# Kernel tuning notes

Measured on AMD Instinct MI355X. Metric: run time of the kernel, lower is better.

Reference implementation:

```python
import jax, jax.numpy as jnp
import numpy as np

D_MODEL = 1024
NUM_HEADS = 16
ROPE_BASE = 10000.0


def _rope_sincos(T, head_dim, dtype):
    # angles[t, i] = t / base**(2i/head_dim), i in [0, head_dim//2)
    pos = jnp.arange(T, dtype=jnp.float32)[:, None]              # [T, 1]
    inv_freq = 1.0 / (ROPE_BASE ** (jnp.arange(0, head_dim, 2, dtype=jnp.float32) / head_dim))
    angles = pos * inv_freq                                       # [T, half]
    sin = jnp.sin(angles).astype(dtype)[None, :, None, :]         # [1, T, 1, half]
    cos = jnp.cos(angles).astype(dtype)[None, :, None, :]
    return sin, cos


def _apply_rope(x, sin, cos):
    # x: [B, T, H, head_dim]; deinterleave even/odd lanes, rotate, concat halves
    x1, x2 = x[..., ::2], x[..., 1::2]                            # [B, T, H, half] each
    return jnp.concatenate([x1 * cos - x2 * sin, x1 * sin + x2 * cos], axis=-1)


def setup_inputs() -> dict:
    key = jax.random.key(0)
    ks = jax.random.split(key, 5)
    B, T, D = 2, 2048, D_MODEL
    s = 0.02
    return {
        "x": jax.random.normal(ks[0], (B, T, D), dtype=jnp.float32),
        "w_qkv": jax.random.normal(ks[1], (3 * D, D), dtype=jnp.float32) * s,
        "b_qkv": jnp.zeros((3 * D,), dtype=jnp.float32),
        "w_out": jax.random.normal(ks[2], (D, D), dtype=jnp.float32) * s,
        "b_out": jnp.zeros((D,), dtype=jnp.float32),
    }


def reference(x, w_qkv, b_qkv, w_out, b_out):
    B, T, D = x.shape
    H = NUM_HEADS
    hd = D // H
    scale = hd ** -0.5

    qkv = (x @ w_qkv.T + b_qkv).reshape(B, T, 3, H, hd)
    q, k, v = qkv[:, :, 0], qkv[:, :, 1], qkv[:, :, 2]            # [B, T, H, hd]

    sin, cos = _rope_sincos(T, hd, x.dtype)
    q = _apply_rope(q, sin, cos)
    k = _apply_rope(k, sin, cos)

    scores = jnp.einsum("bthd,bshd->bhts", q, k) * scale          # [B, H, T, T]
    weights = jax.nn.softmax(scores, axis=-1)
    out = jnp.einsum("bhts,bshd->bthd", weights, v)               # [B, T, H, hd]
    out = out.reshape(B, T, D)
    return out @ w_out.T + b_out
```

## Files before the change

### kernel.cpp

```cpp
#include <hip/hip_runtime.h>
#include <cstdint>
#include <cstddef>

typedef __attribute__((ext_vector_type(8))) short short8;
typedef __attribute__((ext_vector_type(8))) __bf16 bf16x8;
typedef __attribute__((ext_vector_type(4))) float f32x4;
typedef __attribute__((ext_vector_type(16))) float f32x16;
typedef __attribute__((ext_vector_type(4))) unsigned int uint32x4;

#define LOG2E 1.44269504088896340736f

__device__ __forceinline__ unsigned short f2bf(float f) {
    unsigned int u = __builtin_bit_cast(unsigned int, f);
    u += 0x7fffu + ((u >> 16) & 1u);
    return (unsigned short)(u >> 16);
}

__device__ __forceinline__ f32x4 zero4() {
    f32x4 z; z.x = 0.f; z.y = 0.f; z.z = 0.f; z.w = 0.f; return z;
}
__device__ __forceinline__ f32x16 zero16() {
    f32x16 z;
    #pragma unroll
    for (int i = 0; i < 16; ++i) z[i] = 0.f;
    return z;
}

__device__ __forceinline__ f32x4 mfma16(short8 a, short8 b, f32x4 c) {
    return __builtin_amdgcn_mfma_f32_16x16x32_bf16(
        __builtin_bit_cast(bf16x8, a), __builtin_bit_cast(bf16x8, b), c, 0, 0, 0);
}
__device__ __forceinline__ f32x16 mfma32(short8 a, short8 b, f32x16 c) {
    return __builtin_amdgcn_mfma_f32_32x32x16_bf16(
        __builtin_bit_cast(bf16x8, a), __builtin_bit_cast(bf16x8, b), c, 0, 0, 0);
}

__device__ __forceinline__ unsigned int cvt_pk_bf16(float lo, float hi) {
    unsigned int r;
    asm("v_cvt_pk_bf16_f32 %0, %1, %2" : "=v"(r) : "v"(lo), "v"(hi));
    return r;
}

__device__ __forceinline__ uint2 permswap(unsigned x, unsigned y) {
#if __has_builtin(__builtin_amdgcn_permlane32_swap)
    auto r = __builtin_amdgcn_permlane32_swap(x, y, false, false);
    return make_uint2(r[0], r[1]);
#else
    int lane = threadIdx.x & 63;
    unsigned sy = __shfl_xor(y, 32), sx = __shfl_xor(x, 32);
    return make_uint2((lane < 32) ? x : sy, (lane < 32) ? sx : y);
#endif
}
__device__ __forceinline__ float red_max32(float v) {
    unsigned u = __builtin_bit_cast(unsigned, v);
    uint2 p = permswap(u, u);
    return fmaxf(__builtin_bit_cast(float, p.x), __builtin_bit_cast(float, p.y));
}

__device__ __forceinline__ void gload_lds16(const void* g, void* l, int lane) {
#if __has_builtin(__builtin_amdgcn_global_load_lds)
    __builtin_amdgcn_global_load_lds(
        (const __attribute__((address_space(1))) void*)g,
        (__attribute__((address_space(3))) void*)l, 16, 0, 0);
    (void)lane;
#else
    reinterpret_cast<int4*>(l)[lane] = *reinterpret_cast<const int4*>(g);
#endif
}

__global__ __launch_bounds__(256) void prep_kernel(
    const float* __restrict__ x, const float* __restrict__ wq,
    const float* __restrict__ wo,
    unsigned short* __restrict__ xb, unsigned short* __restrict__ wqb,
    unsigned short* __restrict__ wob, float2* __restrict__ tab) {
    const int S0 = 1048576, S1 = 786432, S2 = 262144;
    int i = blockIdx.x * 256 + threadIdx.x;
    const float* src; unsigned short* dst; int j;
    if (i < S0) { src = x; dst = xb; j = i; }
    else if (i < S0 + S1) { src = wq; dst = wqb; j = i - S0; }
    else if (i < S0 + S1 + S2) { src = wo; dst = wob; j = i - S0 - S1; }
    else {
        int idx = i - (S0 + S1 + S2);
        if (idx < 2048 * 32) {
            int t = idx >> 5, ii = idx & 31;
            float inv_freq = powf(10000.0f, -(float)ii / 32.0f);
            float ang = (float)t * inv_freq;
            tab[idx] = make_float2(cosf(ang), sinf(ang));
        }
        return;
    }
    float4 v = reinterpret_cast<const float4*>(src)[j];
    ushort4 o;
    o.x = f2bf(v.x); o.y = f2bf(v.y); o.z = f2bf(v.z); o.w = f2bf(v.w);
    reinterpret_cast<ushort4*>(dst)[j] = o;
}

template<int BM, int BN, int WMG, int WNG>
__device__ __forceinline__ void gemm_mainloop(
    const unsigned short* __restrict__ A, const unsigned short* __restrict__ B,
    int K, int m0, int n0, char* As, char* Bs,
    f32x4 (&acc)[BM / (WMG * 16)][BN / (WNG * 16)]) {
    constexpr int MT = BM / (WMG * 16), NTT = BN / (WNG * 16);
    constexpr int CA = BM / 64, CB = BN / 64;
    constexpr int ABUF = BM * 128, BBUF = BN * 128;
    int tid = threadIdx.x;
    int wave = tid >> 6, lane = tid & 63;
    int wm = wave / WNG, wn = wave % WNG;
    int g = lane >> 4, c = lane & 15;
    const int NS = K >> 6;

    auto stage = [&](int buf, int k0) {
        #pragma unroll
        for (int i = 0; i < CA; ++i) {
            int call = wave * CA + i;
            int s = call * 64 + lane;
            int row = s >> 3, c8 = s & 7;
            int csw = (c8 ^ (row & 7)) << 3;
            gload_lds16(A + (size_t)(m0 + row) * K + k0 + csw,
                        As + buf * ABUF + call * 1024, lane);
        }
        #pragma unroll
        for (int i = 0; i < CB; ++i) {
            int call = wave * CB + i;
            int s = call * 64 + lane;
            int row = s >> 3, c8 = s & 7;
            int csw = (c8 ^ (row & 7)) << 3;
            gload_lds16(B + (size_t)(n0 + row) * K + k0 + csw,
                        Bs + buf * BBUF + call * 1024, lane);
        }
    };

    stage(0, 0);

    #pragma unroll 1
    for (int t = 0; t < NS; ++t) {
        int cur = t & 1;
        asm volatile("s_waitcnt vmcnt(0)" ::: "memory");
        __builtin_amdgcn_s_barrier();
        __builtin_amdgcn_sched_barrier(0);
        if (t + 1 < NS) stage(cur ^ 1, (t + 1) * 64);

        const char* Ac = As + cur * ABUF;
        const char* Bc = Bs + cur * BBUF;
        #pragma unroll
        for (int kg = 0; kg < 2; ++kg) {
            short8 af[MT], bfr[NTT];
            #pragma unroll
            for (int mt = 0; mt < MT; ++mt) {
                int row = wm * (BM / WMG) + mt * 16 + c;
                af[mt] = *reinterpret_cast<const short8*>(Ac +
                    ((row * 128 + kg * 64 + g * 16) ^ ((row & 7) << 4)));
            }
            #pragma unroll
            for (int nt = 0; nt < NTT; ++nt) {
                int row = wn * (BN / WNG) + nt * 16 + c;
                bfr[nt] = *reinterpret_cast<const short8*>(Bc +
                    ((row * 128 + kg * 64 + g * 16) ^ ((row & 7) << 4)));
            }
            __builtin_amdgcn_s_setprio(1);
            #pragma unroll
            for (int mt = 0; mt < MT; ++mt)
                #pragma unroll
                for (int nt = 0; nt < NTT; ++nt)
                    acc[mt][nt] = mfma16(af[mt], bfr[nt], acc[mt][nt]);
            __builtin_amdgcn_s_setprio(0);
        }
    }
}

__global__ __launch_bounds__(512, 2) void qkv_gemm_kernel(
    const unsigned short* __restrict__ X, const unsigned short* __restrict__ W,
    const float* __restrict__ bias, const float2* __restrict__ tab,
    unsigned short* __restrict__ q, unsigned short* __restrict__ k,
    unsigned short* __restrict__ vt) {
    __shared__ char smem[80 * 1024];
    const int K = 1024;
    const float SCL = 0.125f * LOG2E;
    int flat = blockIdx.x;
    int swzb = (flat & 7) * 64 + (flat >> 3);
    int m0 = (swzb >> 4) * 128, n0 = (swzb & 15) * 192;
    f32x4 acc[2][6];
    #pragma unroll
    for (int i = 0; i < 2; ++i)
        #pragma unroll
        for (int j = 0; j < 6; ++j) acc[i][j] = zero4();

    gemm_mainloop<128, 192, 4, 2>(X, W, K, m0, n0, smem, smem + 32768, acc);

    int tid = threadIdx.x;
    int wave = tid >> 6, lane = tid & 63;
    int wm = wave >> 1, wn = wave & 1;
    int g = lane >> 4, c = lane & 15;
    int mbase = m0 + wm * 32, nbase = n0 + wn * 96;
    #pragma unroll
    for (int mt = 0; mt < 2; ++mt) {
        #pragma unroll
        for (int nt = 0; nt < 6; ++nt) {
            f32x4 a = acc[mt][nt];
            int n = nbase + nt * 16 + c;
            int s = n >> 10;
            int h = (n >> 6) & 15;
            int d = n & 63;
            float bn = bias[n];
            #pragma unroll
            for (int r = 0; r < 4; ++r) {
                int m = mbase + mt * 16 + g * 4 + r;
                int bb = m >> 11, t = m & 2047;
                float val = a[r] + bn;
                float partner = __shfl_xor(val, 1);
                int bh = bb * 16 + h;
                if (s == 2) {
                    vt[((size_t)bh * 64 + d) * 2048 + t] = f2bf(val);
                } else {
                    int i2 = d >> 1;
                    float2 cs = tab[t * 32 + i2];
                    float outv; int dout;
                    if ((d & 1) == 0) { outv = val * cs.x - partner * cs.y; dout = i2; }
                    else              { outv = partner * cs.y + val * cs.x; dout = 32 + i2; }
                    if (s == 0) outv *= SCL;
                    (s == 0 ? q : k)[((size_t)bh * 2048 + t) * 64 + dout] = f2bf(outv);
                }
            }
        }
    }
}

__global__ __launch_bounds__(512, 2) void attn_kernel(
    const unsigned short* __restrict__ Q, const unsigned short* __restrict__ Kin,
    const unsigned short* __restrict__ VT, unsigned short* __restrict__ O) {
    __shared__ int4 smem4[65536 / 16];
    char* smem = (char*)smem4;
    const int T = 2048, NT = 16;
    int flat = blockIdx.x + 16 * blockIdx.y;
    int swzb = (flat & 7) * 64 + (flat >> 3);
    int bh = swzb >> 4;
    int qt = swzb & 15;
    int tid = threadIdx.x, wave = tid >> 6, lane = tid & 63;
    int lam = lane & 31, hi = lane >> 5;
    int pair = wave & 3, half = wave >> 2;
    int q = qt * 128 + pair * 32 + lam;

    const unsigned short* Qb = Q + ((size_t)bh * T + q) * 64;
    const unsigned short* Kb = Kin + (size_t)bh * T * 64;
    const unsigned short* VTb = VT + (size_t)bh * 64 * T;

    uint32x4 qtmp[4];
    #pragma unroll
    for (int c4 = 0; c4 < 4; ++c4)
        qtmp[c4] = *reinterpret_cast<const uint32x4*>(Qb + c4 * 16 + hi * 8);
    #pragma unroll
    for (int c4 = 0; c4 < 4; ++c4)
        asm volatile("" : "+v"(qtmp[c4]));
    short8 qf[4];
    #pragma unroll
    for (int c4 = 0; c4 < 4; ++c4) qf[c4] = __builtin_bit_cast(short8, qtmp[c4]);

    short8 ones;
    #pragma unroll
    for (int i = 0; i < 8; ++i) ones[i] = (short)0x3F80;

    f32x16 o0 = zero16(), o1 = zero16(), lacc = zero16();
    float m_run = -1e30f;
    int swz = (lam & 7) << 4;

    char* Ks0 = smem + half * 16384;
    char* Vs0 = smem + 32768 + half * 16384;

    auto stage = [&](int buf, int t) {
        int j0 = half * 1024 + t * 64;
        #pragma unroll
        for (int i = 0; i < 2; ++i) {
            int call = pair * 2 + i;
            int s = call * 64 + lane;
            int row = s >> 3, c8 = s & 7;
            int csw = (c8 ^ (row & 7)) << 3;
            gload_lds16(Kb + (size_t)(j0 + row) * 64 + csw,
                        Ks0 + buf * 8192 + call * 1024, lane);
            gload_lds16(VTb + (size_t)row * T + j0 + csw,
                        Vs0 + buf * 8192 + call * 1024, lane);
        }
    };

    stage(0, 0);

    #pragma unroll 1
    for (int t = 0; t < NT; ++t) {
        int cur = t & 1;
        asm volatile("s_waitcnt vmcnt(0)" ::: "memory");
        __builtin_amdgcn_s_barrier();
        __builtin_amdgcn_sched_barrier(0);
        if (t + 1 < NT) stage(cur ^ 1, t + 1);

        const char* Kc = Ks0 + cur * 8192;
        const char* Vc = Vs0 + cur * 8192;

        f32x16 s0 = zero16(), s1 = zero16();
        __builtin_amdgcn_s_setprio(1);
        #pragma unroll
        for (int c4 = 0; c4 < 4; ++c4) {
            int col = c4 * 32 + hi * 16;
            short8 kf0 = *reinterpret_cast<const short8*>(Kc + ((lam * 128 + col) ^ swz));
            s0 = mfma32(kf0, qf[c4], s0);
            short8 kf1 = *reinterpret_cast<const short8*>(Kc + (((lam + 32) * 128 + col) ^ swz));
            s1 = mfma32(kf1, qf[c4], s1);
        }
        __builtin_amdgcn_s_setprio(0);

        float tm = fmaxf(s0[0], s1[0]);
        #pragma unroll
        for (int r = 1; r < 16; ++r) tm = fmaxf(tm, fmaxf(s0[r], s1[r]));
        float tmax = red_max32(tm);
        if (__any(tmax - m_run > 8.0f)) {
            float mnew = fmaxf(m_run, tmax);
            float alpha = exp2f(m_run - mnew);
            m_run = mnew;
            #pragma unroll
            for (int r = 0; r < 16; ++r) {
                o0[r] *= alpha; o1[r] *= alpha; lacc[r] *= alpha;
            }
        }
        float p0[16], p1[16];
        #pragma unroll
        for (int r = 0; r < 16; ++r) p0[r] = exp2f(s0[r] - m_run);
        #pragma unroll
        for (int r = 0; r < 16; ++r) p1[r] = exp2f(s1[r] - m_run);

        short8 pa[4];
        #pragma unroll
        for (int blk = 0; blk < 2; ++blk) {
            const float* p = blk ? p1 : p0;
            #pragma unroll
            for (int jt = 0; jt < 2; ++jt) {
                unsigned a0 = cvt_pk_bf16(p[jt * 8 + 0], p[jt * 8 + 1]);
                unsigned a1 = cvt_pk_bf16(p[jt * 8 + 2], p[jt * 8 + 3]);
                unsigned b0 = cvt_pk_bf16(p[jt * 8 + 4], p[jt * 8 + 5]);
                unsigned b1 = cvt_pk_bf16(p[jt * 8 + 6], p[jt * 8 + 7]);
                uint2 pr0 = permswap(a0, b0);
                uint2 pr1 = permswap(a1, b1);
                uint4 w;
                w.x = pr0.x;
                w.y = pr1.x;
                w.z = pr0.y;
                w.w = pr1.y;
                pa[blk * 2 + jt] = __builtin_bit_cast(short8, w);
            }
        }

        __builtin_amdgcn_s_setprio(1);
        #pragma unroll
        for (int jt = 0; jt < 4; ++jt) {
            int col = jt * 32 + hi * 16;
            short8 vf0 = *reinterpret_cast<const short8*>(Vc + ((lam * 128 + col) ^ swz));
            o0 = mfma32(vf0, pa[jt], o0);
            short8 vf1 = *reinterpret_cast<const short8*>(Vc + (((lam + 32) * 128 + col) ^ swz));
            o1 = mfma32(vf1, pa[jt], o1);
            lacc = mfma32(ones, pa[jt], lacc);
        }
        __builtin_amdgcn_s_setprio(0);
    }

    float l_run = lacc[0];

    __syncthreads();
    float* pb = (float*)(smem + pair * 8704);
    if (half) {
        #pragma unroll
        for (int r = 0; r < 16; ++r) {
            pb[lane * 34 + r] = o0[r];
            pb[lane * 34 + 16 + r] = o1[r];
        }
        pb[lane * 34 + 32] = m_run;
        pb[lane * 34 + 33] = l_run;
    }
    __syncthreads();
    if (half) return;

    float mb = pb[lane * 34 + 32], lb = pb[lane * 34 + 33];
    float m = fmaxf(m_run, mb);
    float wa = exp2f(m_run - m), wb = exp2f(mb - m);
    float l = l_run * wa + lb * wb;
    float rinv = 1.0f / l;
    #pragma unroll
    for (int r = 0; r < 16; ++r) {
        o0[r] = o0[r] * wa + pb[lane * 34 + r] * wb;
        o1[r] = o1[r] * wa + pb[lane * 34 + 16 + r] * wb;
    }

    int b_ = bh >> 4, h_ = bh & 15;
    unsigned short* Orow = O + ((size_t)(b_ * 2048) + q) * 1024 + h_ * 64;
    #pragma unroll
    for (int rq = 0; rq < 4; ++rq) {
        ushort4 w0, w1;
        w0.x = f2bf(o0[rq * 4 + 0] * rinv);
        w0.y = f2bf(o0[rq * 4 + 1] * rinv);
        w0.z = f2bf(o0[rq * 4 + 2] * rinv);
        w0.w = f2bf(o0[rq * 4 + 3] * rinv);
        w1.x = f2bf(o1[rq * 4 + 0] * rinv);
        w1.y = f2bf(o1[rq * 4 + 1] * rinv);
        w1.z = f2bf(o1[rq * 4 + 2] * rinv);
        w1.w = f2bf(o1[rq * 4 + 3] * rinv);
        int d0 = rq * 8 + hi * 4;
        *reinterpret_cast<ushort4*>(Orow + d0) = w0;
        *reinterpret_cast<ushort4*>(Orow + 32 + d0) = w1;
    }
}

__global__ __launch_bounds__(512, 2) void out_gemm_kernel(
    const unsigned short* __restrict__ Aattn, const unsigned short* __restrict__ W,
    const float* __restrict__ bias, float* __restrict__ out) {
    __shared__ char smem[48 * 1024];
    const int K = 1024, N = 1024;
    int flat = blockIdx.x;
    int swzb = (flat & 7) * 64 + (flat >> 3);
    int m0 = (swzb & 63) * 64, n0 = (swzb >> 6) * 128;
    f32x4 acc[2][2];
    #pragma unroll
    for (int i = 0; i < 2; ++i)
        #pragma unroll
        for (int j = 0; j < 2; ++j) acc[i][j] = zero4();

    gemm_mainloop<64, 128, 2, 4>(Aattn, W, K, m0, n0, smem, smem + 16384, acc);

    int tid = threadIdx.x;
    int wave = tid >> 6, lane = tid & 63;
    int wm = wave >> 2, wn = wave & 3;
    int g = lane >> 4, c = lane & 15;
    int mbase = m0 + wm * 32, nbase = n0 + wn * 32;
    #pragma unroll
    for (int mt = 0; mt < 2; ++mt)
        #pragma unroll
        for (int nt = 0; nt < 2; ++nt) {
            int n = nbase + nt * 16 + c;
            float bn = bias[n];
            #pragma unroll
            for (int r = 0; r < 4; ++r) {
                int m = mbase + mt * 16 + g * 4 + r;
                out[(size_t)m * N + n] = acc[mt][nt][r] + bn;
            }
        }
}

extern "C" void kernel_launch(void* const* d_in, const int* in_sizes, int n_in,
                              void* d_out, int out_size, void* d_ws, size_t ws_size,
                              hipStream_t stream) {
    (void)in_sizes; (void)n_in; (void)out_size; (void)ws_size;
    const float* x     = (const float*)d_in[0];
    const float* w_qkv = (const float*)d_in[1];
    const float* b_qkv = (const float*)d_in[2];
    const float* w_out = (const float*)d_in[3];
    const float* b_out = (const float*)d_in[4];
    float* out = (float*)d_out;

    const int B = 2, T = 2048, D = 1024;
    const int M = B * T;
    const size_t MB = 1024 * 1024;
    (void)D; (void)M;

    char* ws = (char*)d_ws;
    unsigned short* xb    = (unsigned short*)(ws);
    unsigned short* wqkvb = (unsigned short*)(ws + 8 * MB);
    unsigned short* woutb = (unsigned short*)(ws + 14 * MB);
    unsigned short* qb    = (unsigned short*)(ws + 16 * MB);
    unsigned short* kb    = (unsigned short*)(ws + 24 * MB);
    unsigned short* vtb   = (unsigned short*)(ws + 32 * MB);
    unsigned short* attnb = (unsigned short*)(ws + 40 * MB);
    float2* tab           = (float2*)(ws + 48 * MB);

    prep_kernel<<<dim3((2097152 + 65536) / 256), dim3(256), 0, stream>>>(
        x, w_qkv, w_out, xb, wqkvb, woutb, tab);
    qkv_gemm_kernel<<<dim3(512), dim3(512), 0, stream>>>(xb, wqkvb, b_qkv, tab, qb, kb, vtb);
    attn_kernel<<<dim3(T / 128, B * 16), dim3(512), 0, stream>>>(qb, kb, vtb, attnb);
    out_gemm_kernel<<<dim3(512), dim3(512), 0, stream>>>(attnb, woutb, b_out, out);
}
```

Baseline: 143.9 us.

## Drop KV split across wave halves; use 4 waves processing full KV sequence

The attention kernel previously used 8 waves, with two halves each covering half of the key/value sequence, and then merged the partial softmax states through shared memory. It now uses 4 waves per block. Each wave walks the full sequence in 128-key tiles, handled as two 64-key subtiles, so the cross-half merge and its extra barriers go away. In exchange, each block has half the waves and each wave does twice the sequential work, which reduces latency hiding unless occupancy makes up for it.

```diff
diff --git a/kernel.cpp b/kernel.cpp
--- a/kernel.cpp
+++ b/kernel.cpp
@@ -225,7 +225,7 @@
     }
 }
 
-__global__ __launch_bounds__(512, 2) void attn_kernel(
+__global__ __launch_bounds__(256, 2) void attn_kernel(
     const unsigned short* __restrict__ Q, const unsigned short* __restrict__ Kin,
     const unsigned short* __restrict__ VT, unsigned short* __restrict__ O) {
     __shared__ int4 smem4[65536 / 16];
@@ -237,8 +237,7 @@
     int qt = swzb & 15;
     int tid = threadIdx.x, wave = tid >> 6, lane = tid & 63;
     int lam = lane & 31, hi = lane >> 5;
-    int pair = wave & 3, half = wave >> 2;
-    int q = qt * 128 + pair * 32 + lam;
+    int q = qt * 128 + wave * 32 + lam;
 
     const unsigned short* Qb = Q + ((size_t)bh * T + q) * 64;
     const unsigned short* Kb = Kin + (size_t)bh * T * 64;
@@ -263,37 +262,28 @@
     float m_run = -1e30f;
     int swz = (lam & 7) << 4;
 
-    char* Ks0 = smem + half * 16384;
-    char* Vs0 = smem + 32768 + half * 16384;
+    char* KsB = smem;
+    char* VsB = smem + 32768;
 
     auto stage = [&](int buf, int t) {
-        int j0 = half * 1024 + t * 64;
-        #pragma unroll
-        for (int i = 0; i < 2; ++i) {
-            int call = pair * 2 + i;
-            int s = call * 64 + lane;
-            int row = s >> 3, c8 = s & 7;
-            int csw = (c8 ^ (row & 7)) << 3;
-            gload_lds16(Kb + (size_t)(j0 + row) * 64 + csw,
-                        Ks0 + buf * 8192 + call * 1024, lane);
-            gload_lds16(VTb + (size_t)row * T + j0 + csw,
-                        Vs0 + buf * 8192 + call * 1024, lane);
+        int j0 = t * 128;
+        #pragma unroll
+        for (int st = 0; st < 2; ++st) {
+            #pragma unroll
+            for (int i = 0; i < 2; ++i) {
+                int call = wave * 2 + i;
+                int s = call * 64 + lane;
+                int row = s >> 3, c8 = s & 7;
+                int csw = (c8 ^ (row & 7)) << 3;
+                gload_lds16(Kb + (size_t)(j0 + st * 64 + row) * 64 + csw,
+                            KsB + buf * 16384 + st * 8192 + call * 1024, lane);
+                gload_lds16(VTb + (size_t)row * T + j0 + st * 64 + csw,
+                            VsB + buf * 16384 + st * 8192 + call * 1024, lane);
+            }
         }
     };
 
-    stage(0, 0);
-
-    #pragma unroll 1
-    for (int t = 0; t < NT; ++t) {
-        int cur = t & 1;
-        asm volatile("s_waitcnt vmcnt(0)" ::: "memory");
-        __builtin_amdgcn_s_barrier();
-        __builtin_amdgcn_sched_barrier(0);
-        if (t + 1 < NT) stage(cur ^ 1, t + 1);
-
-        const char* Kc = Ks0 + cur * 8192;
-        const char* Vc = Vs0 + cur * 8192;
-
+    auto subtile = [&](const char* Kc, const char* Vc) {
         f32x16 s0 = zero16(), s1 = zero16();
         __builtin_amdgcn_s_setprio(1);
         #pragma unroll
@@ -357,35 +347,25 @@
             lacc = mfma32(ones, pa[jt], lacc);
         }
         __builtin_amdgcn_s_setprio(0);
+    };
+
+    stage(0, 0);
+
+    #pragma unroll 1
+    for (int t = 0; t < NT; ++t) {
+        int cur = t & 1;
+        asm volatile("s_waitcnt vmcnt(0)" ::: "memory");
+        __builtin_amdgcn_s_barrier();
+        __builtin_amdgcn_sched_barrier(0);
+        if (t + 1 < NT) stage(cur ^ 1, t + 1);
+
+        subtile(KsB + cur * 16384, VsB + cur * 16384);
+        subtile(KsB + cur * 16384 + 8192, VsB + cur * 16384 + 8192);
     }
 
     float l_run = lacc[0];
 
-    __syncthreads();
-    float* pb = (float*)(smem + pair * 8704);
-    if (half) {
-        #pragma unroll
-        for (int r = 0; r < 16; ++r) {
-            pb[lane * 34 + r] = o0[r];
-            pb[lane * 34 + 16 + r] = o1[r];
-        }
-        pb[lane * 34 + 32] = m_run;
-        pb[lane * 34 + 33] = l_run;
-    }
-    __syncthreads();
-    if (half) return;
-
-    float mb = pb[lane * 34 + 32], lb = pb[lane * 34 + 33];
-    float m = fmaxf(m_run, mb);
-    float wa = exp2f(m_run - m), wb = exp2f(mb - m);
-    float l = l_run * wa + lb * wb;
-    float rinv = 1.0f / l;
-    #pragma unroll
-    for (int r = 0; r < 16; ++r) {
-        o0[r] = o0[r] * wa + pb[lane * 34 + r] * wb;
-        o1[r] = o1[r] * wa + pb[lane * 34 + 16 + r] * wb;
-    }
-
+    float rinv = 1.0f / l_run;
     int b_ = bh >> 4, h_ = bh & 15;
     unsigned short* Orow = O + ((size_t)(b_ * 2048) + q) * 1024 + h_ * 64;
     #pragma unroll
@@ -469,6 +449,6 @@
     prep_kernel<<<dim3((2097152 + 65536) / 256), dim3(256), 0, stream>>>(
         x, w_qkv, w_out, xb, wqkvb, woutb, tab);
     qkv_gemm_kernel<<<dim3(512), dim3(512), 0, stream>>>(xb, wqkvb, b_qkv, tab, qb, kb, vtb);
-    attn_kernel<<<dim3(T / 128, B * 16), dim3(512), 0, stream>>>(qb, kb, vtb, attnb);
+    attn_kernel<<<dim3(T / 128, B * 16), dim3(256), 0, stream>>>(qb, kb, vtb, attnb);
     out_gemm_kernel<<<dim3(512), dim3(512), 0, stream>>>(attnb, woutb, b_out, out);
 }
```

Result: faster. 140.1 us (-2.6%).
